# Kernel optimization log

Hardware: AMD Instinct MI355X
Metric: run time of the kernel (lower is better)

## Reference

```python
import jax, jax.numpy as jnp
from jax import lax
import numpy as np

NSAMPLE = 32  # from __init__


def setup_inputs() -> dict:
    key = jax.random.key(0)
    k1, k2 = jax.random.split(key)
    B, N, C = 8, 16384, 128
    xyz = jax.random.uniform(k1, (B, N, 3), dtype=jnp.float32)
    points = jax.random.normal(k2, (B, N, C), dtype=jnp.float32)
    return {"npoint": 1024, "radius": 0.2, "xyz": xyz, "points": points}


def furthest_point_sample(xyz, npoint):
    # xyz: (B, N, 3) -> (B, npoint) int32 indices; CUDA impl seeds at index 0
    B, N, _ = xyz.shape
    d0 = jnp.full((B, N), 1e10, dtype=xyz.dtype)
    far0 = jnp.zeros((B,), dtype=jnp.int32)
    barange = jnp.arange(B)

    def step(carry, _):
        d, far = carry
        centroid = xyz[barange, far]                      # (B, 3)
        dist = jnp.sum((xyz - centroid[:, None, :]) ** 2, axis=-1)  # (B, N)
        d = jnp.minimum(d, dist)
        far_new = jnp.argmax(d, axis=-1).astype(jnp.int32)
        return (d, far_new), far

    _, idxs = lax.scan(step, (d0, far0), None, length=npoint)
    return idxs.T  # (B, npoint)


def ball_query(radius, nsample, xyz, new_xyz):
    # returns idx (B, S, nsample): first <=nsample point indices within radius,
    # remaining slots filled with the first found index (0 if none found)
    B, N, _ = xyz.shape
    S = new_xyz.shape[1]
    # squared distances via GEMM to avoid (B,S,N,3) temp
    d2 = (jnp.sum(new_xyz ** 2, -1)[:, :, None]
          + jnp.sum(xyz ** 2, -1)[:, None, :]
          - 2.0 * jnp.einsum('bsd,bnd->bsn', new_xyz, xyz))  # (B, S, N)
    mask = d2 < radius * radius
    arangeN = jnp.arange(N, dtype=jnp.int32)
    key = jnp.where(mask, arangeN, N)                 # invalid -> sentinel N
    neg_vals, pos = lax.top_k(-key, nsample)          # smallest keys first
    valid = (-neg_vals) < N                           # (B, S, nsample)
    first = pos[..., 0:1]
    fill = jnp.where(valid[..., 0:1], first, 0)
    idx = jnp.where(valid, pos, fill).astype(jnp.int32)
    return idx


def _group(feat, idx):
    # feat: (B, N, C), idx: (B, S, K) -> (B, S, K, C)
    return jax.vmap(lambda f, i: f[i])(feat, idx)


def reference(npoint, radius, xyz, points):
    fps_idx = furthest_point_sample(xyz, npoint)              # (B, npoint)
    new_xyz = jax.vmap(lambda x, i: x[i])(xyz, fps_idx)       # (B, npoint, 3)
    idx = ball_query(radius, NSAMPLE, xyz, new_xyz)           # (B, npoint, K)
    grouped_xyz = _group(xyz, idx) - new_xyz[:, :, None, :]   # (B, npoint, K, 3)
    new_points = _group(points, idx)                          # use_xyz=False
    return new_xyz, new_points, idx, grouped_xyz
```

## Files before the change

### kernel.cpp

```cpp
#include <hip/hip_runtime.h>

#define B 8
#define N 16384
#define NPOINT 1024
#define NSAMPLE 32
#define CDIM 128
#define CELLS 4096
#define NSEG 1024
#define FT 512

#define OFF_NEWXYZ 0
#define OFF_NEWPTS (B * NPOINT * 3)
#define OFF_IDX    (OFF_NEWPTS + B * NPOINT * NSAMPLE * CDIM)
#define OFF_GXYZ   (OFF_IDX + B * NPOINT * NSAMPLE)

typedef unsigned long long u64;

template <int CTRL>
__device__ __forceinline__ u64 mindpp_u64(u64 k) {
    const int lo = (int)(unsigned)(k & 0xffffffffull);
    const int hi = (int)(unsigned)(k >> 32);
    const int lo2 = __builtin_amdgcn_update_dpp(lo, lo, CTRL, 0xf, 0xf, false);
    const int hi2 = __builtin_amdgcn_update_dpp(hi, hi, CTRL, 0xf, 0xf, false);
    const u64 kt = ((u64)(unsigned)hi2 << 32) | (unsigned)lo2;
    return kt < k ? kt : k;
}

__device__ __forceinline__ int spread3(int v) {
    return (v & 1) | ((v & 2) << 2) | ((v & 4) << 4) | ((v & 8) << 6);
}

__global__ __launch_bounds__(1024) void sort_kernel(const float* __restrict__ xyz,
                                                    float* __restrict__ sorted) {
    const int b = blockIdx.x;
    const int t = threadIdx.x;
    const float* xb = xyz + (size_t)b * N * 3;

    __shared__ unsigned int hist[CELLS];
    __shared__ unsigned int waveS[16];

#pragma unroll
    for (int i = 0; i < CELLS / 1024; ++i) hist[i * 1024 + t] = 0;
    __syncthreads();

    int cell[16];
#pragma unroll
    for (int k = 0; k < 16; ++k) {
        const int n = k * 1024 + t;
        const float x = xb[n * 3 + 0];
        const float y = xb[n * 3 + 1];
        const float z = xb[n * 3 + 2];
        int cx = (int)(x * 16.0f); cx = cx < 0 ? 0 : (cx > 15 ? 15 : cx);
        int cy = (int)(y * 16.0f); cy = cy < 0 ? 0 : (cy > 15 ? 15 : cy);
        int cz = (int)(z * 16.0f); cz = cz < 0 ? 0 : (cz > 15 ? 15 : cz);
        cell[k] = spread3(cx) | (spread3(cy) << 1) | (spread3(cz) << 2);
        atomicAdd(&hist[cell[k]], 1u);
    }
    __syncthreads();

    const unsigned h0 = hist[4 * t + 0], h1 = hist[4 * t + 1],
                   h2 = hist[4 * t + 2], h3 = hist[4 * t + 3];
    const unsigned sum4 = h0 + h1 + h2 + h3;
    const int wid = t >> 6, lane = t & 63;
    unsigned inc = sum4;
#pragma unroll
    for (int off = 1; off < 64; off <<= 1) {
        const unsigned v = __shfl_up(inc, off);
        if (lane >= off) inc += v;
    }
    if (lane == 63) waveS[wid] = inc;
    __syncthreads();
    unsigned wbase = 0;
    {
        unsigned ws = (lane < 16) ? waveS[lane] : 0u;
        unsigned wi = ws;
#pragma unroll
        for (int off = 1; off < 16; off <<= 1) {
            const unsigned v = __shfl_up(wi, off);
            if (lane >= off) wi += v;
        }
        wbase = __shfl(wi - ws, wid);
    }
    const unsigned base = wbase + (inc - sum4);
    __syncthreads();
    hist[4 * t + 0] = base;
    hist[4 * t + 1] = base + h0;
    hist[4 * t + 2] = base + h0 + h1;
    hist[4 * t + 3] = base + h0 + h1 + h2;
    __syncthreads();

    float4* sb = (float4*)sorted + (size_t)b * N;
#pragma unroll
    for (int k = 0; k < 16; ++k) {
        const int n = k * 1024 + t;
        const float x = xb[n * 3 + 0];
        const float y = xb[n * 3 + 1];
        const float z = xb[n * 3 + 2];
        const unsigned pos = atomicAdd(&hist[cell[k]], 1u);
        sb[pos] = make_float4(x, y, z, (float)n);
    }
}

__global__ __launch_bounds__(FT) void fps_kernel(const float* __restrict__ xyz,
                                                 const float* __restrict__ sorted,
                                                 float* out) {
#pragma clang fp contract(off)
    const int b = blockIdx.x;
    const int t = threadIdx.x;
    const float* xb = xyz + (size_t)b * N * 3;
    const float4* sb = (const float4*)sorted + (size_t)b * N;

    __shared__ float sd[N];
    __shared__ u64 segkey[NSEG];
    __shared__ unsigned short queue[NSEG];
    __shared__ unsigned qc[2];
    __shared__ u64 swkey[2][8];

    const int wid = t >> 6;
    const int lane = t & 63;

    float lox0 = 1e30f, hix0 = -1e30f, loy0 = 1e30f, hiy0 = -1e30f, loz0 = 1e30f, hiz0 = -1e30f;
    float lox1 = 1e30f, hix1 = -1e30f, loy1 = 1e30f, hiy1 = -1e30f, loz1 = 1e30f, hiz1 = -1e30f;
#pragma unroll
    for (int k = 0; k < 16; ++k) {
        const float4 v0 = sb[t * 16 + k];
        const float4 v1 = sb[(t + FT) * 16 + k];
        lox0 = fminf(lox0, v0.x); hix0 = fmaxf(hix0, v0.x);
        loy0 = fminf(loy0, v0.y); hiy0 = fmaxf(hiy0, v0.y);
        loz0 = fminf(loz0, v0.z); hiz0 = fmaxf(hiz0, v0.z);
        lox1 = fminf(lox1, v1.x); hix1 = fmaxf(hix1, v1.x);
        loy1 = fminf(loy1, v1.y); hiy1 = fmaxf(hiy1, v1.y);
        loz1 = fminf(loz1, v1.z); hiz1 = fmaxf(hiz1, v1.z);
        sd[t * 16 + k] = 1e10f;
        sd[(t + FT) * 16 + k] = 1e10f;
    }
    if (t < 2) qc[t] = 0;
    u64 rkey0 = ~0ull, rkey1 = ~0ull;
    float mval0 = 1e10f, mval1 = 1e10f;
    __syncthreads();

    float* nxo = out + OFF_NEWXYZ + (size_t)b * NPOINT * 3;
    int far = 0;

    for (int s = 0; s < NPOINT; ++s) {
        const int fs = __builtin_amdgcn_readfirstlane(far);
        const float cx = xb[fs * 3 + 0];
        const float cy = xb[fs * 3 + 1];
        const float cz = xb[fs * 3 + 2];
        if (t == 0) {
            nxo[s * 3 + 0] = cx;
            nxo[s * 3 + 1] = cy;
            nxo[s * 3 + 2] = cz;
        }
        if (s == NPOINT - 1) break;

        const float ax0 = fmaxf(fmaxf(__fsub_rn(lox0, cx), __fsub_rn(cx, hix0)), 0.0f);
        const float ay0 = fmaxf(fmaxf(__fsub_rn(loy0, cy), __fsub_rn(cy, hiy0)), 0.0f);
        const float az0 = fmaxf(fmaxf(__fsub_rn(loz0, cz), __fsub_rn(cz, hiz0)), 0.0f);
        const float md20 = __fadd_rn(__fadd_rn(__fmul_rn(ax0, ax0), __fmul_rn(ay0, ay0)),
                                     __fmul_rn(az0, az0));
        const bool ex0 = !(md20 > __fmul_rn(mval0, 1.0001f));
        const float ax1 = fmaxf(fmaxf(__fsub_rn(lox1, cx), __fsub_rn(cx, hix1)), 0.0f);
        const float ay1 = fmaxf(fmaxf(__fsub_rn(loy1, cy), __fsub_rn(cy, hiy1)), 0.0f);
        const float az1 = fmaxf(fmaxf(__fsub_rn(loz1, cz), __fsub_rn(cz, hiz1)), 0.0f);
        const float md21 = __fadd_rn(__fadd_rn(__fmul_rn(ax1, ax1), __fmul_rn(ay1, ay1)),
                                     __fmul_rn(az1, az1));
        const bool ex1 = !(md21 > __fmul_rn(mval1, 1.0001f));
        if (t == 0) qc[(s + 1) & 1] = 0;
        {
            const u64 bal0 = __ballot(ex0);
            unsigned wb = 0;
            if (lane == 0) wb = atomicAdd(&qc[s & 1], (unsigned)__popcll(bal0));
            wb = __shfl(wb, 0);
            if (ex0) {
                const unsigned pos = wb + (unsigned)__popcll(bal0 & ((1ull << lane) - 1ull));
                queue[pos] = (unsigned short)t;
            }
            const u64 bal1 = __ballot(ex1);
            unsigned wb1 = 0;
            if (lane == 0) wb1 = atomicAdd(&qc[s & 1], (unsigned)__popcll(bal1));
            wb1 = __shfl(wb1, 0);
            if (ex1) {
                const unsigned pos = wb1 + (unsigned)__popcll(bal1 & ((1ull << lane) - 1ull));
                queue[pos] = (unsigned short)(t + FT);
            }
        }
        __syncthreads();

        const unsigned nseg = qc[s & 1];
        const int row = t >> 4;
        const int col = t & 15;
        for (unsigned j = (unsigned)row; j < nseg; j += FT / 16) {
            const int seg = queue[j];
            const int p = (seg << 4) | col;
            const float4 v = sb[p];
            const float dx = __fsub_rn(v.x, cx);
            const float dy = __fsub_rn(v.y, cy);
            const float dz = __fsub_rn(v.z, cz);
            const float dist = __fadd_rn(
                __fadd_rn(__fmul_rn(dx, dx), __fmul_rn(dy, dy)),
                __fmul_rn(dz, dz));
            const float dnew = fminf(sd[p], dist);
            sd[p] = dnew;
            u64 key = ((u64)(unsigned)(~__float_as_uint(dnew)) << 14) |
                      (unsigned)(int)v.w;
            key = mindpp_u64<0x111>(key);
            key = mindpp_u64<0x112>(key);
            key = mindpp_u64<0x114>(key);
            key = mindpp_u64<0x118>(key);
            if (col == 15) segkey[seg] = key;
        }
        __syncthreads();

        if (ex0) {
            const u64 rk = segkey[t];
            rkey0 = rk;
            mval0 = __uint_as_float(~(unsigned)(rk >> 14));
        }
        if (ex1) {
            const u64 rk = segkey[t + FT];
            rkey1 = rk;
            mval1 = __uint_as_float(~(unsigned)(rk >> 14));
        }
        u64 key = rkey0 < rkey1 ? rkey0 : rkey1;
        key = mindpp_u64<0x111>(key);
        key = mindpp_u64<0x112>(key);
        key = mindpp_u64<0x114>(key);
        key = mindpp_u64<0x118>(key);
        key = mindpp_u64<0x142>(key);
        key = mindpp_u64<0x143>(key);
        if (lane == 63) swkey[s & 1][wid] = key;
        __syncthreads();
        u64 kk = swkey[s & 1][lane & 7];
        kk = mindpp_u64<0x111>(kk);
        kk = mindpp_u64<0x112>(kk);
        kk = mindpp_u64<0x114>(kk);
        const int lo7 = __builtin_amdgcn_readlane((int)(unsigned)(kk & 0xffffffffull), 7);
        far = lo7 & 16383;
    }
}

__global__ __launch_bounds__(256) void ballq_kernel(const float* __restrict__ xyz,
                                                    const float* __restrict__ radius_p,
                                                    float* out) {
    const int wib = threadIdx.x >> 6;
    const int lane = threadIdx.x & 63;
    const int gw = blockIdx.x * 4 + wib;
    const int b = gw >> 10;
    const int s = gw & 1023;

    const float r = radius_p[0];
    const float r2 = __fmul_rn(r, r);

    const float* xb = xyz + (size_t)b * N * 3;
    const float* nx = out + OFF_NEWXYZ + (size_t)(b * NPOINT + s) * 3;
    const float c0 = nx[0], c1 = nx[1], c2 = nx[2];
    const float ss_s = __fadd_rn(__fadd_rn(__fmul_rn(c0, c0), __fmul_rn(c1, c1)),
                                 __fmul_rn(c2, c2));

    float* oidx = out + OFF_IDX + (size_t)(b * NPOINT + s) * NSAMPLE;
    float* ogx  = out + OFF_GXYZ + (size_t)(b * NPOINT + s) * NSAMPLE * 3;

    int filled = 0;
    int first = -1;
    for (int n0 = 0; n0 < N; n0 += 64) {
        const int n = n0 + lane;
        const float x = xb[n * 3 + 0];
        const float y = xb[n * 3 + 1];
        const float z = xb[n * 3 + 2];
        const float ssx = __fadd_rn(__fadd_rn(__fmul_rn(x, x), __fmul_rn(y, y)),
                                    __fmul_rn(z, z));
        const float dot = __fadd_rn(__fadd_rn(__fmul_rn(c0, x), __fmul_rn(c1, y)),
                                    __fmul_rn(c2, z));
        const float d2 = __fsub_rn(__fadd_rn(ss_s, ssx), __fmul_rn(2.0f, dot));
        const bool in = d2 < r2;
        const unsigned long long m = __ballot(in);
        if (first < 0 && m != 0ull) first = n0 + (int)__builtin_ctzll(m);
        if (in) {
            const int pos = filled + (int)__popcll(m & ((1ull << lane) - 1ull));
            if (pos < NSAMPLE) {
                oidx[pos] = (float)n;
                ogx[pos * 3 + 0] = __fsub_rn(x, c0);
                ogx[pos * 3 + 1] = __fsub_rn(y, c1);
                ogx[pos * 3 + 2] = __fsub_rn(z, c2);
            }
        }
        filled += (int)__popcll(m);
        if (filled >= NSAMPLE) break;
    }
    if (filled < NSAMPLE) {
        if (first < 0) first = 0;
        const float fx = xb[first * 3 + 0];
        const float fy = xb[first * 3 + 1];
        const float fz = xb[first * 3 + 2];
        const float g0 = __fsub_rn(fx, c0);
        const float g1 = __fsub_rn(fy, c1);
        const float g2 = __fsub_rn(fz, c2);
        for (int pos = filled + lane; pos < NSAMPLE; pos += 64) {
            oidx[pos] = (float)first;
            ogx[pos * 3 + 0] = g0;
            ogx[pos * 3 + 1] = g1;
            ogx[pos * 3 + 2] = g2;
        }
    }
}

__global__ __launch_bounds__(256) void gather_kernel(const float* __restrict__ points,
                                                     float* out) {
    const int blk = blockIdx.x;
    const int w = threadIdx.x >> 6;
    const int lane = threadIdx.x & 63;
    const int b = blk >> 10;

    const float* oidx = out + OFF_IDX + (size_t)blk * NSAMPLE;
    const float* pb = points + (size_t)b * N * CDIM;
    float* onp = out + OFF_NEWPTS + (size_t)blk * NSAMPLE * CDIM;

#pragma unroll
    for (int i = 0; i < 8; ++i) {
        const int slot = w * 8 + i;
        const int n = (int)oidx[slot];
        const float2 v = *(const float2*)(pb + (size_t)n * CDIM + lane * 2);
        *(float2*)(onp + (size_t)slot * CDIM + lane * 2) = v;
    }
}

extern "C" void kernel_launch(void* const* d_in, const int* in_sizes, int n_in,
                              void* d_out, int out_size, void* d_ws, size_t ws_size,
                              hipStream_t stream) {
    const float* xyz = (const float*)d_in[2];
    const float* points = (const float*)d_in[3];
    const float* radius = (const float*)d_in[1];
    float* out = (float*)d_out;

    float* sorted = out + OFF_NEWPTS;

    hipLaunchKernelGGL(sort_kernel, dim3(B), dim3(1024), 0, stream, xyz, sorted);
    hipLaunchKernelGGL(fps_kernel, dim3(B), dim3(FT), 0, stream, xyz, sorted, out);
    hipLaunchKernelGGL(ballq_kernel, dim3((B * NPOINT) / 4), dim3(256), 0, stream, xyz, radius, out);
    hipLaunchKernelGGL(gather_kernel, dim3(B * NPOINT), dim3(256), 0, stream, points, out);
}
```

Baseline: 1.578 ms.

## Process two batches per FPS block with 1024 threads

```diff
diff --git a/kernel.cpp b/kernel.cpp
--- a/kernel.cpp
+++ b/kernel.cpp
@@ -6,8 +6,6 @@
 #define NSAMPLE 32
 #define CDIM 128
 #define CELLS 4096
-#define NSEG 1024
-#define FT 512
 
 #define OFF_NEWXYZ 0
 #define OFF_NEWPTS (B * NPOINT * 3)
@@ -101,20 +99,27 @@
     }
 }
 
-__global__ __launch_bounds__(FT) void fps_kernel(const float* __restrict__ xyz,
-                                                 const float* __restrict__ sorted,
-                                                 float* out) {
+__global__ __launch_bounds__(1024) void fps_kernel(const float* __restrict__ xyz,
+                                                   const float* __restrict__ sorted,
+                                                   float* out) {
 #pragma clang fp contract(off)
-    const int b = blockIdx.x;
+    const int b0 = blockIdx.x * 2;
+    const int b1 = b0 + 1;
     const int t = threadIdx.x;
-    const float* xb = xyz + (size_t)b * N * 3;
-    const float4* sb = (const float4*)sorted + (size_t)b * N;
-
-    __shared__ float sd[N];
-    __shared__ u64 segkey[NSEG];
-    __shared__ unsigned short queue[NSEG];
-    __shared__ unsigned qc[2];
-    __shared__ u64 swkey[2][8];
+    const float* xb0 = xyz + (size_t)b0 * N * 3;
+    const float* xb1 = xyz + (size_t)b1 * N * 3;
+    const float4* sb0 = (const float4*)sorted + (size_t)b0 * N;
+    const float4* sb1 = (const float4*)sorted + (size_t)b1 * N;
+
+    __shared__ float sd0[N];
+    __shared__ float sd1[N];
+    __shared__ u64 segkey0[1024];
+    __shared__ u64 segkey1[1024];
+    __shared__ unsigned short queue0[1024];
+    __shared__ unsigned short queue1[1024];
+    __shared__ unsigned qc[2][2];
+    __shared__ u64 swkey0[2][16];
+    __shared__ u64 swkey1[2][16];
 
     const int wid = t >> 6;
     const int lane = t & 63;
@@ -123,120 +128,154 @@
     float lox1 = 1e30f, hix1 = -1e30f, loy1 = 1e30f, hiy1 = -1e30f, loz1 = 1e30f, hiz1 = -1e30f;
 #pragma unroll
     for (int k = 0; k < 16; ++k) {
-        const float4 v0 = sb[t * 16 + k];
-        const float4 v1 = sb[(t + FT) * 16 + k];
+        const float4 v0 = sb0[t * 16 + k];
+        const float4 v1 = sb1[t * 16 + k];
         lox0 = fminf(lox0, v0.x); hix0 = fmaxf(hix0, v0.x);
         loy0 = fminf(loy0, v0.y); hiy0 = fmaxf(hiy0, v0.y);
         loz0 = fminf(loz0, v0.z); hiz0 = fmaxf(hiz0, v0.z);
         lox1 = fminf(lox1, v1.x); hix1 = fmaxf(hix1, v1.x);
         loy1 = fminf(loy1, v1.y); hiy1 = fmaxf(hiy1, v1.y);
         loz1 = fminf(loz1, v1.z); hiz1 = fmaxf(hiz1, v1.z);
-        sd[t * 16 + k] = 1e10f;
-        sd[(t + FT) * 16 + k] = 1e10f;
-    }
-    if (t < 2) qc[t] = 0;
+        sd0[t * 16 + k] = 1e10f;
+        sd1[t * 16 + k] = 1e10f;
+    }
+    if (t == 0) { qc[0][0] = 0; qc[0][1] = 0; qc[1][0] = 0; qc[1][1] = 0; }
     u64 rkey0 = ~0ull, rkey1 = ~0ull;
     float mval0 = 1e10f, mval1 = 1e10f;
     __syncthreads();
 
-    float* nxo = out + OFF_NEWXYZ + (size_t)b * NPOINT * 3;
-    int far = 0;
+    float* nxo0 = out + OFF_NEWXYZ + (size_t)b0 * NPOINT * 3;
+    float* nxo1 = out + OFF_NEWXYZ + (size_t)b1 * NPOINT * 3;
+    int far0 = 0, far1 = 0;
 
     for (int s = 0; s < NPOINT; ++s) {
-        const int fs = __builtin_amdgcn_readfirstlane(far);
-        const float cx = xb[fs * 3 + 0];
-        const float cy = xb[fs * 3 + 1];
-        const float cz = xb[fs * 3 + 2];
+        const int fs0 = __builtin_amdgcn_readfirstlane(far0);
+        const int fs1 = __builtin_amdgcn_readfirstlane(far1);
+        const float cx0 = xb0[fs0 * 3 + 0];
+        const float cy0 = xb0[fs0 * 3 + 1];
+        const float cz0 = xb0[fs0 * 3 + 2];
+        const float cx1 = xb1[fs1 * 3 + 0];
+        const float cy1 = xb1[fs1 * 3 + 1];
+        const float cz1 = xb1[fs1 * 3 + 2];
         if (t == 0) {
-            nxo[s * 3 + 0] = cx;
-            nxo[s * 3 + 1] = cy;
-            nxo[s * 3 + 2] = cz;
+            nxo0[s * 3 + 0] = cx0;
+            nxo0[s * 3 + 1] = cy0;
+            nxo0[s * 3 + 2] = cz0;
+            nxo1[s * 3 + 0] = cx1;
+            nxo1[s * 3 + 1] = cy1;
+            nxo1[s * 3 + 2] = cz1;
         }
         if (s == NPOINT - 1) break;
 
-        const float ax0 = fmaxf(fmaxf(__fsub_rn(lox0, cx), __fsub_rn(cx, hix0)), 0.0f);
-        const float ay0 = fmaxf(fmaxf(__fsub_rn(loy0, cy), __fsub_rn(cy, hiy0)), 0.0f);
-        const float az0 = fmaxf(fmaxf(__fsub_rn(loz0, cz), __fsub_rn(cz, hiz0)), 0.0f);
+        const float ax0 = fmaxf(fmaxf(__fsub_rn(lox0, cx0), __fsub_rn(cx0, hix0)), 0.0f);
+        const float ay0 = fmaxf(fmaxf(__fsub_rn(loy0, cy0), __fsub_rn(cy0, hiy0)), 0.0f);
+        const float az0 = fmaxf(fmaxf(__fsub_rn(loz0, cz0), __fsub_rn(cz0, hiz0)), 0.0f);
         const float md20 = __fadd_rn(__fadd_rn(__fmul_rn(ax0, ax0), __fmul_rn(ay0, ay0)),
                                      __fmul_rn(az0, az0));
         const bool ex0 = !(md20 > __fmul_rn(mval0, 1.0001f));
-        const float ax1 = fmaxf(fmaxf(__fsub_rn(lox1, cx), __fsub_rn(cx, hix1)), 0.0f);
-        const float ay1 = fmaxf(fmaxf(__fsub_rn(loy1, cy), __fsub_rn(cy, hiy1)), 0.0f);
-        const float az1 = fmaxf(fmaxf(__fsub_rn(loz1, cz), __fsub_rn(cz, hiz1)), 0.0f);
+        const float ax1 = fmaxf(fmaxf(__fsub_rn(lox1, cx1), __fsub_rn(cx1, hix1)), 0.0f);
+        const float ay1 = fmaxf(fmaxf(__fsub_rn(loy1, cy1), __fsub_rn(cy1, hiy1)), 0.0f);
+        const float az1 = fmaxf(fmaxf(__fsub_rn(loz1, cz1), __fsub_rn(cz1, hiz1)), 0.0f);
         const float md21 = __fadd_rn(__fadd_rn(__fmul_rn(ax1, ax1), __fmul_rn(ay1, ay1)),
                                      __fmul_rn(az1, az1));
         const bool ex1 = !(md21 > __fmul_rn(mval1, 1.0001f));
-        if (t == 0) qc[(s + 1) & 1] = 0;
+        if (t == 0) { qc[(s + 1) & 1][0] = 0; qc[(s + 1) & 1][1] = 0; }
         {
             const u64 bal0 = __ballot(ex0);
-            unsigned wb = 0;
-            if (lane == 0) wb = atomicAdd(&qc[s & 1], (unsigned)__popcll(bal0));
-            wb = __shfl(wb, 0);
+            unsigned wb0 = 0;
+            if (lane == 0) wb0 = atomicAdd(&qc[s & 1][0], (unsigned)__popcll(bal0));
+            wb0 = __shfl(wb0, 0);
             if (ex0) {
-                const unsigned pos = wb + (unsigned)__popcll(bal0 & ((1ull << lane) - 1ull));
-                queue[pos] = (unsigned short)t;
+                const unsigned pos = wb0 + (unsigned)__popcll(bal0 & ((1ull << lane) - 1ull));
+                queue0[pos] = (unsigned short)t;
             }
             const u64 bal1 = __ballot(ex1);
             unsigned wb1 = 0;
-            if (lane == 0) wb1 = atomicAdd(&qc[s & 1], (unsigned)__popcll(bal1));
+            if (lane == 0) wb1 = atomicAdd(&qc[s & 1][1], (unsigned)__popcll(bal1));
             wb1 = __shfl(wb1, 0);
             if (ex1) {
                 const unsigned pos = wb1 + (unsigned)__popcll(bal1 & ((1ull << lane) - 1ull));
-                queue[pos] = (unsigned short)(t + FT);
+                queue1[pos] = (unsigned short)t;
             }
         }
         __syncthreads();
 
-        const unsigned nseg = qc[s & 1];
+        const unsigned nseg0 = qc[s & 1][0];
+        const unsigned nseg1 = qc[s & 1][1];
         const int row = t >> 4;
         const int col = t & 15;
-        for (unsigned j = (unsigned)row; j < nseg; j += FT / 16) {
-            const int seg = queue[j];
+        for (unsigned j = (unsigned)row; j < nseg0; j += 64) {
+            const int seg = queue0[j];
             const int p = (seg << 4) | col;
-            const float4 v = sb[p];
-            const float dx = __fsub_rn(v.x, cx);
-            const float dy = __fsub_rn(v.y, cy);
-            const float dz = __fsub_rn(v.z, cz);
+            const float4 v = sb0[p];
+            const float dx = __fsub_rn(v.x, cx0);
+            const float dy = __fsub_rn(v.y, cy0);
+            const float dz = __fsub_rn(v.z, cz0);
             const float dist = __fadd_rn(
                 __fadd_rn(__fmul_rn(dx, dx), __fmul_rn(dy, dy)),
                 __fmul_rn(dz, dz));
-            const float dnew = fminf(sd[p], dist);
-            sd[p] = dnew;
+            const float dnew = fminf(sd0[p], dist);
+            sd0[p] = dnew;
             u64 key = ((u64)(unsigned)(~__float_as_uint(dnew)) << 14) |
                       (unsigned)(int)v.w;
             key = mindpp_u64<0x111>(key);
             key = mindpp_u64<0x112>(key);
             key = mindpp_u64<0x114>(key);
             key = mindpp_u64<0x118>(key);
-            if (col == 15) segkey[seg] = key;
+            if (col == 15) segkey0[seg] = key;
+        }
+        for (unsigned j = (unsigned)row; j < nseg1; j += 64) {
+            const int seg = queue1[j];
+            const int p = (seg << 4) | col;
+            const float4 v = sb1[p];
+            const float dx = __fsub_rn(v.x, cx1);
+            const float dy = __fsub_rn(v.y, cy1);
+            const float dz = __fsub_rn(v.z, cz1);
+            const float dist = __fadd_rn(
+                __fadd_rn(__fmul_rn(dx, dx), __fmul_rn(dy, dy)),
+                __fmul_rn(dz, dz));
+            const float dnew = fminf(sd1[p], dist);
+            sd1[p] = dnew;
+            u64 key = ((u64)(unsigned)(~__float_as_uint(dnew)) << 14) |
+                      (unsigned)(int)v.w;
+            key = mindpp_u64<0x111>(key);
+            key = mindpp_u64<0x112>(key);
+            key = mindpp_u64<0x114>(key);
+            key = mindpp_u64<0x118>(key);
+            if (col == 15) segkey1[seg] = key;
         }
         __syncthreads();
 
         if (ex0) {
-            const u64 rk = segkey[t];
+            const u64 rk = segkey0[t];
             rkey0 = rk;
             mval0 = __uint_as_float(~(unsigned)(rk >> 14));
         }
         if (ex1) {
-            const u64 rk = segkey[t + FT];
+            const u64 rk = segkey1[t];
             rkey1 = rk;
             mval1 = __uint_as_float(~(unsigned)(rk >> 14));
         }
-        u64 key = rkey0 < rkey1 ? rkey0 : rkey1;
-        key = mindpp_u64<0x111>(key);
-        key = mindpp_u64<0x112>(key);
-        key = mindpp_u64<0x114>(key);
-        key = mindpp_u64<0x118>(key);
-        key = mindpp_u64<0x142>(key);
-        key = mindpp_u64<0x143>(key);
-        if (lane == 63) swkey[s & 1][wid] = key;
+        u64 k0 = rkey0, k1 = rkey1;
+        k0 = mindpp_u64<0x111>(k0);  k1 = mindpp_u64<0x111>(k1);
+        k0 = mindpp_u64<0x112>(k0);  k1 = mindpp_u64<0x112>(k1);
+        k0 = mindpp_u64<0x114>(k0);  k1 = mindpp_u64<0x114>(k1);
+        k0 = mindpp_u64<0x118>(k0);  k1 = mindpp_u64<0x118>(k1);
+        k0 = mindpp_u64<0x142>(k0);  k1 = mindpp_u64<0x142>(k1);
+        k0 = mindpp_u64<0x143>(k0);  k1 = mindpp_u64<0x143>(k1);
+        if (lane == 63) {
+            swkey0[s & 1][wid] = k0;
+            swkey1[s & 1][wid] = k1;
+        }
         __syncthreads();
-        u64 kk = swkey[s & 1][lane & 7];
-        kk = mindpp_u64<0x111>(kk);
-        kk = mindpp_u64<0x112>(kk);
-        kk = mindpp_u64<0x114>(kk);
-        const int lo7 = __builtin_amdgcn_readlane((int)(unsigned)(kk & 0xffffffffull), 7);
-        far = lo7 & 16383;
+        u64 kk0 = swkey0[s & 1][lane & 15];
+        u64 kk1 = swkey1[s & 1][lane & 15];
+        kk0 = mindpp_u64<0x111>(kk0);  kk1 = mindpp_u64<0x111>(kk1);
+        kk0 = mindpp_u64<0x112>(kk0);  kk1 = mindpp_u64<0x112>(kk1);
+        kk0 = mindpp_u64<0x114>(kk0);  kk1 = mindpp_u64<0x114>(kk1);
+        kk0 = mindpp_u64<0x118>(kk0);  kk1 = mindpp_u64<0x118>(kk1);
+        far0 = __builtin_amdgcn_readlane((int)(unsigned)(kk0 & 0xffffffffull), 15) & 16383;
+        far1 = __builtin_amdgcn_readlane((int)(unsigned)(kk1 & 0xffffffffull), 15) & 16383;
     }
 }
 
@@ -336,7 +375,7 @@
     float* sorted = out + OFF_NEWPTS;
 
     hipLaunchKernelGGL(sort_kernel, dim3(B), dim3(1024), 0, stream, xyz, sorted);
-    hipLaunchKernelGGL(fps_kernel, dim3(B), dim3(FT), 0, stream, xyz, sorted, out);
+    hipLaunchKernelGGL(fps_kernel, dim3(B / 2), dim3(1024), 0, stream, xyz, sorted, out);
     hipLaunchKernelGGL(ballq_kernel, dim3((B * NPOINT) / 4), dim3(256), 0, stream, xyz, radius, out);
     hipLaunchKernelGGL(gather_kernel, dim3(B * NPOINT), dim3(256), 0, stream, points, out);
 }
```

Result: slower. 2.647 ms (+67.7%).
